# Kernel tuning notes

Hardware: AMD Instinct MI355X
Metric: run time of the kernel (lower is better)

## Reference

```python
import jax, jax.numpy as jnp
import numpy as np
from jax import lax

B, T, D = 1, 2048, 2048
H, KVH, HD = 16, 4, 128
BETA = 0.9
ROPE_BASE = 10000.0


def _causal_prefix_ema(x, beta):
    # x: (B, T, D); m_t = beta * m_{t-1} + (1 - beta) * x_t, m_{-1} = 0
    def step(m, xt):
        m = beta * m + (1.0 - beta) * xt
        return m, m
    _, ys = lax.scan(step, jnp.zeros_like(x[:, 0]), jnp.swapaxes(x, 0, 1))
    return jnp.swapaxes(ys, 0, 1)


def _rotate_half(x):
    x1, x2 = jnp.split(x, 2, axis=-1)
    return jnp.concatenate([-x2, x1], axis=-1)


def _rope_cos_sin(t, hd, dtype):
    inv_freq = 1.0 / (ROPE_BASE ** (jnp.arange(0, hd, 2, dtype=jnp.float32) / hd))
    freqs = jnp.arange(t, dtype=jnp.float32)[:, None] * inv_freq[None, :]  # (T, HD/2)
    emb = jnp.concatenate([freqs, freqs], axis=-1)  # (T, HD)
    return jnp.cos(emb).astype(dtype)[None, None], jnp.sin(emb).astype(dtype)[None, None]


def setup_inputs() -> dict:
    key = jax.random.key(0)
    ks = jax.random.split(key, 8)
    std = 0.02
    return {
        "hidden_states": jax.random.normal(ks[0], (B, T, D), jnp.float32),
        "Wq": jax.random.normal(ks[1], (D, H * HD), jnp.float32) * std,
        "Wk": jax.random.normal(ks[2], (D, KVH * HD), jnp.float32) * std,
        "Wv": jax.random.normal(ks[3], (D, KVH * HD), jnp.float32) * std,
        "Wo": jax.random.normal(ks[4], (H * HD, D), jnp.float32) * std,
        "Wr1": jax.random.normal(ks[5], (D, D // 2), jnp.float32) * std,
        "br1": jnp.zeros((D // 2,), jnp.float32),
        "Wr2": jax.random.normal(ks[6], (D // 2, 2), jnp.float32) * std,
        "br2": jnp.zeros((2,), jnp.float32),
    }


def reference(hidden_states, Wq, Wk, Wv, Wo, Wr1, br1, Wr2, br2):
    b, t, d = hidden_states.shape
    q = hidden_states @ Wq  # (B, T, H*HD)

    # multi-level memories: l1 = raw, l2 = causal prefix EMA
    l2 = _causal_prefix_ema(hidden_states, BETA)

    # router MLP on q + softmax over levels
    h = jax.nn.silu(q @ Wr1 + br1)
    lam = jax.nn.softmax(h @ Wr2 + br2, axis=-1)  # (B, T, 2)
    fused = lam[..., 0:1] * hidden_states + lam[..., 1:2] * l2

    # shape to heads
    q_s = q.reshape(b, t, H, HD).transpose(0, 2, 1, 3)                 # (B, H, T, HD)
    k_s = (fused @ Wk).reshape(b, t, KVH, HD).transpose(0, 2, 1, 3)    # (B, KVH, T, HD)
    v_s = (fused @ Wv).reshape(b, t, KVH, HD).transpose(0, 2, 1, 3)

    # RoPE
    cos, sin = _rope_cos_sin(t, HD, q_s.dtype)
    q_s = q_s * cos + _rotate_half(q_s) * sin
    k_s = k_s * cos + _rotate_half(k_s) * sin

    # repeat kv for GQA
    n_rep = H // KVH
    k_s = jnp.repeat(k_s, n_rep, axis=1)
    v_s = jnp.repeat(v_s, n_rep, axis=1)

    # causal SDPA
    scale = 1.0 / jnp.sqrt(jnp.asarray(HD, q_s.dtype))
    scores = jnp.einsum("bhqd,bhkd->bhqk", q_s, k_s) * scale
    causal = jnp.tril(jnp.ones((t, t), dtype=bool))
    scores = jnp.where(causal[None, None], scores, jnp.finfo(scores.dtype).min)
    attn = jax.nn.softmax(scores, axis=-1)
    out = jnp.einsum("bhqk,bhkd->bhqd", attn, v_s)  # (B, H, T, HD)

    out = out.transpose(0, 2, 1, 3).reshape(b, t, H * HD)
    return out @ Wo
```

## Files before the change

### kernel.cpp

```cpp
#include <hip/hip_runtime.h>
#include <hip/hip_bf16.h>

#define T_SEQ 2048
#define D_MODEL 2048
#define NH 16
#define NKVH 4
#define HD 128

typedef __attribute__((ext_vector_type(8))) short bf16x8;
typedef __attribute__((ext_vector_type(4))) float f32x4;

static __device__ __forceinline__ short f32_to_bf16(float f) {
    unsigned u = __float_as_uint(f);
    u += 0x7fffu + ((u >> 16) & 1u);
    return (short)(u >> 16);
}
static __device__ __forceinline__ float bf16_to_f32(short s) {
    return __uint_as_float(((unsigned)(unsigned short)s) << 16);
}
static __device__ __forceinline__ void gl_to_lds16(const void* g, void* l) {
    __builtin_amdgcn_global_load_lds(
        (const __attribute__((address_space(1))) unsigned int*)g,
        (__attribute__((address_space(3))) unsigned int*)l, 16, 0, 0);
}

template<int BN>
__global__ __launch_bounds__(256, 2) void gemm_bt_kernel(
    const short* __restrict__ A, const short* __restrict__ Bt,
    float* __restrict__ Cf, short* __restrict__ Cb,
    int M, int N, int K, const float* __restrict__ bias, int act)
{
    constexpr int NI = BN / 64;
    constexpr int BCH = BN / 32;
    __shared__ short Alds[2][64 * 64];
    __shared__ short Blds[2][BN * 64];

    const int tid = threadIdx.x;
    const int wave = tid >> 6, lane = tid & 63;
    const int l16 = lane & 15, quad = lane >> 4;
    const int wn = wave * (BN / 4);
    const int m0 = blockIdx.y * 64, n0 = blockIdx.x * BN;
    const int niter = K >> 6;

    f32x4 acc[4][NI] = {};

    #pragma unroll
    for (int p = 0; p < 2; ++p) {
        int li = p * 256 + tid;
        int row = li >> 3, sc = li & 7;
        gl_to_lds16(A + (size_t)(m0 + row) * K + ((sc ^ (row & 7)) * 8),
                    &Alds[0][(size_t)(p * 256 + wave * 64) * 8]);
    }
    #pragma unroll
    for (int p = 0; p < BCH; ++p) {
        int li = p * 256 + tid;
        int row = li >> 3, sc = li & 7;
        gl_to_lds16(Bt + (size_t)(n0 + row) * K + ((sc ^ (row & 7)) * 8),
                    &Blds[0][(size_t)(p * 256 + wave * 64) * 8]);
    }

    for (int t = 0; t < niter; ++t) {
        asm volatile("s_waitcnt vmcnt(0)\n\ts_barrier" ::: "memory");

        if (t + 1 < niter) {
            int k1 = (t + 1) << 6;
            int nb = (t + 1) & 1;
            #pragma unroll
            for (int p = 0; p < 2; ++p) {
                int li = p * 256 + tid;
                int row = li >> 3, sc = li & 7;
                gl_to_lds16(A + (size_t)(m0 + row) * K + k1 + ((sc ^ (row & 7)) * 8),
                            &Alds[nb][(size_t)(p * 256 + wave * 64) * 8]);
            }
            #pragma unroll
            for (int p = 0; p < BCH; ++p) {
                int li = p * 256 + tid;
                int row = li >> 3, sc = li & 7;
                gl_to_lds16(Bt + (size_t)(n0 + row) * K + k1 + ((sc ^ (row & 7)) * 8),
                            &Blds[nb][(size_t)(p * 256 + wave * 64) * 8]);
            }
        }

        const short* Ab = Alds[t & 1];
        const short* Bb = Blds[t & 1];
        #pragma unroll
        for (int kk = 0; kk < 2; ++kk) {
            bf16x8 a[4], b[NI];
            #pragma unroll
            for (int i = 0; i < 4; ++i)
                a[i] = *(const bf16x8*)
                    &Ab[(size_t)(i * 16 + l16) * 64 + (((kk * 4 + quad) ^ (l16 & 7)) * 8)];
            #pragma unroll
            for (int i = 0; i < NI; ++i)
                b[i] = *(const bf16x8*)
                    &Bb[(size_t)(wn + i * 16 + l16) * 64 + (((kk * 4 + quad) ^ (l16 & 7)) * 8)];
            #pragma unroll
            for (int mi = 0; mi < 4; ++mi)
                #pragma unroll
                for (int ni = 0; ni < NI; ++ni)
                    acc[mi][ni] = __builtin_amdgcn_mfma_f32_16x16x32_bf16(
                        a[mi], b[ni], acc[mi][ni], 0, 0, 0);
        }
    }

    #pragma unroll
    for (int mi = 0; mi < 4; ++mi) {
        #pragma unroll
        for (int ni = 0; ni < NI; ++ni) {
            int col = n0 + wn + ni * 16 + l16;
            float bv = bias ? bias[col] : 0.0f;
            #pragma unroll
            for (int r = 0; r < 4; ++r) {
                int row = m0 + mi * 16 + quad * 4 + r;
                float x = acc[mi][ni][r] + bv;
                if (act) x = x / (1.0f + __expf(-x));
                size_t o = (size_t)row * N + col;
                if (Cf) Cf[o] = x;
                if (Cb) Cb[o] = f32_to_bf16(x);
            }
        }
    }
}

__global__ __launch_bounds__(256) void transpose_all_kernel(
    const float* __restrict__ Wq, const float* __restrict__ Wk,
    const float* __restrict__ Wv, const float* __restrict__ Wr1,
    const float* __restrict__ Wo, short* __restrict__ Wq_t,
    short* __restrict__ Wkv_t, short* __restrict__ Wr1_t,
    short* __restrict__ Wo_t)
{
    __shared__ float tile[32][33];
    int bx = blockIdx.x;
    const float* src; short* dst; int ld, cb;
    if (bx < 64)       { src = Wq;  dst = Wq_t;  ld = 2048; cb = bx; }
    else if (bx < 80)  { src = Wk;  dst = Wkv_t; ld = 512;  cb = bx - 64; }
    else if (bx < 96)  { src = Wv;  dst = Wkv_t + (size_t)512 * 2048; ld = 512; cb = bx - 80; }
    else if (bx < 128) { src = Wr1; dst = Wr1_t; ld = 1024; cb = bx - 96; }
    else               { src = Wo;  dst = Wo_t;  ld = 2048; cb = bx - 128; }
    int c0 = cb * 32, r0 = blockIdx.y * 32;
    int t = threadIdx.x;
    int r = t >> 3, c4 = (t & 7) * 4;
    float4 v = *(const float4*)&src[(size_t)(r0 + r) * ld + c0 + c4];
    tile[r][c4 + 0] = v.x; tile[r][c4 + 1] = v.y;
    tile[r][c4 + 2] = v.z; tile[r][c4 + 3] = v.w;
    __syncthreads();
    short o[4];
    #pragma unroll
    for (int j = 0; j < 4; ++j) o[j] = f32_to_bf16(tile[c4 + j][r]);
    *(uint2*)&dst[(size_t)(c0 + r) * 2048 + r0 + c4] = *(const uint2*)o;
}

__global__ __launch_bounds__(256) void transpose_bf_kernel(
    const short* __restrict__ src, int ld, short* __restrict__ dst, int ldd)
{
    __shared__ float tile[32][33];
    int r0 = blockIdx.y * 32, c0 = blockIdx.x * 32;
    int x = threadIdx.x & 31, y = threadIdx.x >> 5;
    #pragma unroll
    for (int i = 0; i < 4; ++i)
        tile[y + i * 8][x] = bf16_to_f32(src[(size_t)(r0 + y + i * 8) * ld + c0 + x]);
    __syncthreads();
    #pragma unroll
    for (int i = 0; i < 4; ++i)
        dst[(size_t)(c0 + y + i * 8) * ldd + r0 + x] = f32_to_bf16(tile[x][y + i * 8]);
}

__global__ __launch_bounds__(256) void ema_kernel(const float* __restrict__ hs,
                                                  float* __restrict__ l2,
                                                  short* __restrict__ hs_b)
{
    int d = blockIdx.y * 256 + threadIdx.x;
    int t0 = blockIdx.x * 128;
    int ts = t0 - 192; if (ts < 0) ts = 0;
    float m = 0.0f;
    for (int tb = ts; tb < t0; tb += 16) {
        float buf[16];
        #pragma unroll
        for (int j = 0; j < 16; ++j) buf[j] = hs[(size_t)(tb + j) * D_MODEL + d];
        #pragma unroll
        for (int j = 0; j < 16; ++j) m = 0.9f * m + 0.1f * buf[j];
    }
    for (int tb = t0; tb < t0 + 128; tb += 16) {
        float buf[16];
        #pragma unroll
        for (int j = 0; j < 16; ++j) buf[j] = hs[(size_t)(tb + j) * D_MODEL + d];
        #pragma unroll
        for (int j = 0; j < 16; ++j) hs_b[(size_t)(tb + j) * D_MODEL + d] = f32_to_bf16(buf[j]);
        #pragma unroll
        for (int j = 0; j < 16; ++j) { m = 0.9f * m + 0.1f * buf[j]; buf[j] = m; }
        #pragma unroll
        for (int j = 0; j < 16; ++j) l2[(size_t)(tb + j) * D_MODEL + d] = buf[j];
    }
}

__global__ __launch_bounds__(64) void lam_kernel(
    const short* __restrict__ h, const float* __restrict__ Wr2,
    const float* __restrict__ br2, float* __restrict__ lam)
{
    int t = blockIdx.x;
    int lane = threadIdx.x;
    float z0 = 0.0f, z1 = 0.0f;
    for (int i = lane; i < 1024; i += 64) {
        float hv = bf16_to_f32(h[(size_t)t * 1024 + i]);
        z0 += hv * Wr2[i * 2 + 0];
        z1 += hv * Wr2[i * 2 + 1];
    }
    #pragma unroll
    for (int off = 1; off < 64; off <<= 1) {
        z0 += __shfl_xor(z0, off);
        z1 += __shfl_xor(z1, off);
    }
    if (lane == 0) {
        z0 += br2[0]; z1 += br2[1];
        float mx = fmaxf(z0, z1);
        float e0 = expf(z0 - mx), e1 = expf(z1 - mx);
        float inv = 1.0f / (e0 + e1);
        lam[t * 2 + 0] = e0 * inv;
        lam[t * 2 + 1] = e1 * inv;
    }
}

__global__ void fuse_kernel(const float* __restrict__ hs, const float* __restrict__ l2,
                            const float* __restrict__ lam, short* __restrict__ fused)
{
    int idx = blockIdx.x * blockDim.x + threadIdx.x;
    int t = idx >> 9;
    float a0 = lam[t * 2 + 0], a1 = lam[t * 2 + 1];
    float4 a = ((const float4*)hs)[idx];
    float4 b = ((const float4*)l2)[idx];
    short o[4] = {f32_to_bf16(a0 * a.x + a1 * b.x), f32_to_bf16(a0 * a.y + a1 * b.y),
                  f32_to_bf16(a0 * a.z + a1 * b.z), f32_to_bf16(a0 * a.w + a1 * b.w)};
    *(uint2*)(fused + (size_t)idx * 4) = *(const uint2*)o;
}

__global__ void rope_q_kernel(const short* __restrict__ q, short* __restrict__ qr)
{
    int idx = blockIdx.x * blockDim.x + threadIdx.x;
    int d = idx & 63;
    int h = (idx >> 6) & 15;
    int t = idx >> 10;
    float fr = (float)t * __expf(-(float)d * 0.14391156831212787f);
    float s, c;
    sincosf(fr, &s, &c);
    const float sc = 0.08838834764831845f;
    const short* src = q + (size_t)t * D_MODEL + h * HD;
    float x1 = bf16_to_f32(src[d]) * sc, x2 = bf16_to_f32(src[d + 64]) * sc;
    short* dst = qr + ((size_t)h * T_SEQ + t) * HD;
    dst[d]      = f32_to_bf16(x1 * c - x2 * s);
    dst[d + 64] = f32_to_bf16(x2 * c + x1 * s);
}

__global__ void rope_k_kernel(const short* __restrict__ kv, short* __restrict__ kr)
{
    int idx = blockIdx.x * blockDim.x + threadIdx.x;
    int d = idx & 63;
    int kh = (idx >> 6) & 3;
    int t = idx >> 8;
    float fr = (float)t * __expf(-(float)d * 0.14391156831212787f);
    float s, c;
    sincosf(fr, &s, &c);
    const short* src = kv + (size_t)t * 1024 + kh * HD;
    float x1 = bf16_to_f32(src[d]), x2 = bf16_to_f32(src[d + 64]);
    short* dst = kr + ((size_t)kh * T_SEQ + t) * HD;
    dst[d]      = f32_to_bf16(x1 * c - x2 * s);
    dst[d + 64] = f32_to_bf16(x2 * c + x1 * s);
}

__global__ __launch_bounds__(512, 2) void attn_kernel(
    const short* __restrict__ Qr, const short* __restrict__ Kr,
    const short* __restrict__ Vt, short* __restrict__ Out)
{
    const int h = blockIdx.x;
    const int qt = blockIdx.y;
    const int kvh = h >> 2;
    const int tid = threadIdx.x;
    const int wave = tid >> 6, lane = tid & 63;
    const int l16 = lane & 15, quad = lane >> 4;
    const int wq = wave & 3;
    const int wk = wave >> 2;

    __shared__ __align__(16) char smem[163840];
    short* Klds = (short*)smem;
    short* Vlds = (short*)(smem + 65536);
    short* Plds = (short*)(smem + 131072);

    const short* kbase = Kr + (size_t)kvh * T_SEQ * HD;
    const short* vbase = Vt + (size_t)kvh * HD * T_SEQ;

    const int qbase = qt * 128 + wq * 32;
    const int ko = wk * 64;
    const int n = qt + 1;

    bf16x8 qf[2][4];
    #pragma unroll
    for (int m = 0; m < 2; ++m) {
        const short* qrow = Qr + ((size_t)h * T_SEQ + qbase + m * 16 + l16) * HD;
        #pragma unroll
        for (int kc = 0; kc < 4; ++kc)
            qf[m][kc] = *(const bf16x8*)&qrow[kc * 32 + quad * 8];
    }
    f32x4 o[2][8] = {};
    float lsum[2][4] = {};

    {
        #pragma unroll
        for (int p = 0; p < 4; ++p) {
            int li = p * 512 + tid;
            int row = li >> 4, gs = (li & 15) ^ (row & 15);
            gl_to_lds16(kbase + (size_t)row * HD + gs * 8,
                        &Klds[(size_t)(p * 512 + wave * 64) * 8]);
        }
        #pragma unroll
        for (int p = 0; p < 4; ++p) {
            int li = p * 512 + tid;
            int row = li >> 4, gs = (li & 15) ^ (row & 15);
            gl_to_lds16(vbase + (size_t)row * T_SEQ + gs * 8,
                        &Vlds[(size_t)(p * 512 + wave * 64) * 8]);
        }
    }

    for (int t = 0; t < n; ++t) {
        asm volatile("s_waitcnt vmcnt(0)\n\ts_barrier" ::: "memory");

        if (t + 1 < n) {
            int kv1 = (t + 1) << 7;
            int nb = (t + 1) & 1;
            const short* ks = kbase + (size_t)kv1 * HD;
            #pragma unroll
            for (int p = 0; p < 4; ++p) {
                int li = p * 512 + tid;
                int row = li >> 4, gs = (li & 15) ^ (row & 15);
                gl_to_lds16(ks + (size_t)row * HD + gs * 8,
                            &Klds[(size_t)(nb * 16384 + (p * 512 + wave * 64) * 8)]);
            }
            #pragma unroll
            for (int p = 0; p < 4; ++p) {
                int li = p * 512 + tid;
                int row = li >> 4, gs = (li & 15) ^ (row & 15);
                gl_to_lds16(vbase + (size_t)row * T_SEQ + kv1 + gs * 8,
                            &Vlds[(size_t)(nb * 16384 + (p * 512 + wave * 64) * 8)]);
            }
        }

        const short* Kb = Klds + (size_t)(t & 1) * 16384;
        const short* Vb = Vlds + (size_t)(t & 1) * 16384;

        f32x4 s[2][4];
        #pragma unroll
        for (int m = 0; m < 2; ++m)
            #pragma unroll
            for (int ni = 0; ni < 4; ++ni) s[m][ni] = (f32x4){0, 0, 0, 0};
        __builtin_amdgcn_s_setprio(1);
        #pragma unroll
        for (int ni = 0; ni < 4; ++ni)
            #pragma unroll
            for (int kc = 0; kc < 4; ++kc) {
                bf16x8 b = *(const bf16x8*)
                    &Kb[(size_t)(ko + ni * 16 + l16) * 128 + (((kc * 4 + quad) ^ l16) * 8)];
                s[0][ni] = __builtin_amdgcn_mfma_f32_16x16x32_bf16(qf[0][kc], b, s[0][ni], 0, 0, 0);
                s[1][ni] = __builtin_amdgcn_mfma_f32_16x16x32_bf16(qf[1][kc], b, s[1][ni], 0, 0, 0);
            }
        __builtin_amdgcn_s_setprio(0);

        if (t == n - 1) {
            int kvg0 = (t << 7) + ko;
            #pragma unroll
            for (int m = 0; m < 2; ++m)
                #pragma unroll
                for (int ni = 0; ni < 4; ++ni) {
                    int kvg = kvg0 + ni * 16 + l16;
                    #pragma unroll
                    for (int r = 0; r < 4; ++r) {
                        int qg = qbase + m * 16 + quad * 4 + r;
                        float p = (kvg <= qg) ? __expf(s[m][ni][r]) : 0.0f;
                        lsum[m][r] += p;
                        int prow = quad * 4 + r, pcol = ni * 16 + l16;
                        Plds[wave * 2048 + (m * 16 + prow) * 64 +
                             (((pcol >> 3) ^ (prow & 7)) * 8) + (pcol & 7)] = f32_to_bf16(p);
                    }
                }
        } else {
            #pragma unroll
            for (int m = 0; m < 2; ++m)
                #pragma unroll
                for (int ni = 0; ni < 4; ++ni)
                    #pragma unroll
                    for (int r = 0; r < 4; ++r) {
                        float p = __expf(s[m][ni][r]);
                        lsum[m][r] += p;
                        int prow = quad * 4 + r, pcol = ni * 16 + l16;
                        Plds[wave * 2048 + (m * 16 + prow) * 64 +
                             (((pcol >> 3) ^ (prow & 7)) * 8) + (pcol & 7)] = f32_to_bf16(p);
                    }
        }
        asm volatile("s_waitcnt lgkmcnt(0)" ::: "memory");

        __builtin_amdgcn_s_setprio(1);
        #pragma unroll
        for (int kc = 0; kc < 2; ++kc) {
            bf16x8 pa0 = *(const bf16x8*)
                &Plds[wave * 2048 + l16 * 64 + (((kc * 4 + quad) ^ (l16 & 7)) * 8)];
            bf16x8 pa1 = *(const bf16x8*)
                &Plds[wave * 2048 + (16 + l16) * 64 + (((kc * 4 + quad) ^ (l16 & 7)) * 8)];
            #pragma unroll
            for (int d8 = 0; d8 < 8; ++d8) {
                bf16x8 b = *(const bf16x8*)
                    &Vb[(size_t)(d8 * 16 + l16) * 128 +
                        (((wk * 8 + kc * 4 + quad) ^ l16) * 8)];
                o[0][d8] = __builtin_amdgcn_mfma_f32_16x16x32_bf16(pa0, b, o[0][d8], 0, 0, 0);
                o[1][d8] = __builtin_amdgcn_mfma_f32_16x16x32_bf16(pa1, b, o[1][d8], 0, 0, 0);
            }
        }
        __builtin_amdgcn_s_setprio(0);
    }

    __syncthreads();
    float* Ox = (float*)smem;
    float* Lx = (float*)(smem + 67584);
    if (wk) {
        #pragma unroll
        for (int m = 0; m < 2; ++m)
            #pragma unroll
            for (int d8 = 0; d8 < 8; ++d8)
                #pragma unroll
                for (int r = 0; r < 4; ++r)
                    Ox[(wq * 32 + m * 16 + quad * 4 + r) * 132 + d8 * 16 + l16] = o[m][d8][r];
        #pragma unroll
        for (int m = 0; m < 2; ++m)
            #pragma unroll
            for (int r = 0; r < 4; ++r)
                Lx[(wq * 32 + m * 16 + quad * 4 + r) * 16 + l16] = lsum[m][r];
    }
    __syncthreads();
    if (!wk) {
        #pragma unroll
        for (int m = 0; m < 2; ++m)
            #pragma unroll
            for (int d8 = 0; d8 < 8; ++d8)
                #pragma unroll
                for (int r = 0; r < 4; ++r)
                    o[m][d8][r] += Ox[(wq * 32 + m * 16 + quad * 4 + r) * 132 + d8 * 16 + l16];
        #pragma unroll
        for (int m = 0; m < 2; ++m)
            #pragma unroll
            for (int r = 0; r < 4; ++r) {
                lsum[m][r] += Lx[(wq * 32 + m * 16 + quad * 4 + r) * 16 + l16];
                #pragma unroll
                for (int off = 1; off < 16; off <<= 1)
                    lsum[m][r] += __shfl_xor(lsum[m][r], off);
                lsum[m][r] = 1.0f / lsum[m][r];
            }
        #pragma unroll
        for (int m = 0; m < 2; ++m)
            #pragma unroll
            for (int d8 = 0; d8 < 8; ++d8)
                #pragma unroll
                for (int r = 0; r < 4; ++r) {
                    int row = qbase + m * 16 + quad * 4 + r;
                    Out[(size_t)row * D_MODEL + h * HD + d8 * 16 + l16] =
                        f32_to_bf16(o[m][d8][r] * lsum[m][r]);
                }
    }
}

extern "C" void kernel_launch(void* const* d_in, const int* in_sizes, int n_in,
                              void* d_out, int out_size, void* d_ws, size_t ws_size,
                              hipStream_t stream)
{
    const float* hs  = (const float*)d_in[0];
    const float* Wq  = (const float*)d_in[1];
    const float* Wk  = (const float*)d_in[2];
    const float* Wv  = (const float*)d_in[3];
    const float* Wo  = (const float*)d_in[4];
    const float* Wr1 = (const float*)d_in[5];
    const float* br1 = (const float*)d_in[6];
    const float* Wr2 = (const float*)d_in[7];
    const float* br2 = (const float*)d_in[8];
    float* out = (float*)d_out;

    char* w = (char*)d_ws;
    const size_t MB = 1u << 20;
    float* l2_f     = (float*)(w + 0 * MB);
    short* hs_bf    = (short*)(w + 16 * MB);
    short* Wq_t     = (short*)(w + 24 * MB);
    short* Wkv_t    = (short*)(w + 32 * MB);
    short* Wr1_t    = (short*)(w + 36 * MB);
    short* Wo_t     = (short*)(w + 40 * MB);
    short* q_bf     = (short*)(w + 48 * MB);
    short* h_bf     = (short*)(w + 56 * MB);
    short* fused_bf = (short*)(w + 60 * MB);
    short* kv_bf    = (short*)(w + 68 * MB);
    short* qr       = (short*)(w + 72 * MB);
    short* kr       = (short*)(w + 80 * MB);
    short* vr       = (short*)(w + 82 * MB);
    float* lam_f    = (float*)(w + 84 * MB);
    short* attn_bf  = hs_bf;

    transpose_all_kernel<<<dim3(192, 64), 256, 0, stream>>>(
        Wq, Wk, Wv, Wr1, Wo, Wq_t, Wkv_t, Wr1_t, Wo_t);

    ema_kernel<<<dim3(T_SEQ / 128, D_MODEL / 256), 256, 0, stream>>>(hs, l2_f, hs_bf);

    gemm_bt_kernel<128><<<dim3(16, 32), 256, 0, stream>>>(
        hs_bf, Wq_t, nullptr, q_bf, 2048, 2048, 2048, nullptr, 0);

    gemm_bt_kernel<64><<<dim3(16, 32), 256, 0, stream>>>(
        q_bf, Wr1_t, nullptr, h_bf, 2048, 1024, 2048, br1, 1);

    lam_kernel<<<T_SEQ, 64, 0, stream>>>(h_bf, Wr2, br2, lam_f);

    fuse_kernel<<<(T_SEQ * D_MODEL / 4) / 256, 256, 0, stream>>>(hs, l2_f, lam_f, fused_bf);

    gemm_bt_kernel<64><<<dim3(16, 32), 256, 0, stream>>>(
        fused_bf, Wkv_t, nullptr, kv_bf, 2048, 1024, 2048, nullptr, 0);

    rope_q_kernel<<<(T_SEQ * NH * 64) / 256, 256, 0, stream>>>(q_bf, qr);
    rope_k_kernel<<<(T_SEQ * NKVH * 64) / 256, 256, 0, stream>>>(kv_bf, kr);
    transpose_bf_kernel<<<dim3(16, 64), 256, 0, stream>>>(kv_bf + 512, 1024, vr, 2048);

    attn_kernel<<<dim3(NH, 16), 512, 0, stream>>>(qr, kr, vr, attn_bf);

    gemm_bt_kernel<128><<<dim3(16, 32), 256, 0, stream>>>(
        attn_bf, Wo_t, out, nullptr, 2048, 2048, 2048, nullptr, 0);
}
```

Before: 321.6 us.

## Balance causal attention by pairing 64-row query tiles per block

The attention kernel now gives each block two 64-row query tiles, y and 31-y, in sequence, so the causal work per block is roughly equal. Previously each block handled a single 128-row tile, so the work per block grew with the tile index. Waves are reorganised as 2 query groups by 4 KV splits. Partial O and row sums from 3 waves are reduced through LDS, and the LDS footprint is reduced. The cost is that even tiles compute half-masked 128-wide KV blocks, and there is extra reduction and a barrier between phases.

```diff
diff --git a/kernel.cpp b/kernel.cpp
--- a/kernel.cpp
+++ b/kernel.cpp
@@ -271,15 +271,15 @@
     const short* __restrict__ Vt, short* __restrict__ Out)
 {
     const int h = blockIdx.x;
-    const int qt = blockIdx.y;
+    const int y = blockIdx.y;
     const int kvh = h >> 2;
     const int tid = threadIdx.x;
     const int wave = tid >> 6, lane = tid & 63;
     const int l16 = lane & 15, quad = lane >> 4;
-    const int wq = wave & 3;
-    const int wk = wave >> 2;
-
-    __shared__ __align__(16) char smem[163840];
+    const int wq = wave & 1;
+    const int wk = wave >> 1;
+
+    __shared__ __align__(16) char smem[147456];
     short* Klds = (short*)smem;
     short* Vlds = (short*)(smem + 65536);
     short* Plds = (short*)(smem + 131072);
@@ -287,179 +287,190 @@
     const short* kbase = Kr + (size_t)kvh * T_SEQ * HD;
     const short* vbase = Vt + (size_t)kvh * HD * T_SEQ;
 
-    const int qbase = qt * 128 + wq * 32;
-    const int ko = wk * 64;
-    const int n = qt + 1;
-
-    bf16x8 qf[2][4];
-    #pragma unroll
-    for (int m = 0; m < 2; ++m) {
-        const short* qrow = Qr + ((size_t)h * T_SEQ + qbase + m * 16 + l16) * HD;
-        #pragma unroll
-        for (int kc = 0; kc < 4; ++kc)
-            qf[m][kc] = *(const bf16x8*)&qrow[kc * 32 + quad * 8];
-    }
-    f32x4 o[2][8] = {};
-    float lsum[2][4] = {};
-
-    {
-        #pragma unroll
-        for (int p = 0; p < 4; ++p) {
-            int li = p * 512 + tid;
-            int row = li >> 4, gs = (li & 15) ^ (row & 15);
-            gl_to_lds16(kbase + (size_t)row * HD + gs * 8,
-                        &Klds[(size_t)(p * 512 + wave * 64) * 8]);
-        }
-        #pragma unroll
-        for (int p = 0; p < 4; ++p) {
-            int li = p * 512 + tid;
-            int row = li >> 4, gs = (li & 15) ^ (row & 15);
-            gl_to_lds16(vbase + (size_t)row * T_SEQ + gs * 8,
-                        &Vlds[(size_t)(p * 512 + wave * 64) * 8]);
-        }
-    }
-
-    for (int t = 0; t < n; ++t) {
-        asm volatile("s_waitcnt vmcnt(0)\n\ts_barrier" ::: "memory");
-
-        if (t + 1 < n) {
-            int kv1 = (t + 1) << 7;
-            int nb = (t + 1) & 1;
-            const short* ks = kbase + (size_t)kv1 * HD;
+    #pragma unroll 1
+    for (int ph = 0; ph < 2; ++ph) {
+        const int qt32 = ph ? (31 - y) : y;
+        const int qbase = qt32 * 64 + wq * 32;
+        const int n = (qt32 >> 1) + 1;
+        const int ko = wk * 32;
+
+        bf16x8 qf[2][4];
+        #pragma unroll
+        for (int m = 0; m < 2; ++m) {
+            const short* qrow = Qr + ((size_t)h * T_SEQ + qbase + m * 16 + l16) * HD;
+            #pragma unroll
+            for (int kc = 0; kc < 4; ++kc)
+                qf[m][kc] = *(const bf16x8*)&qrow[kc * 32 + quad * 8];
+        }
+        f32x4 o[2][8] = {};
+        float lsum[2][4] = {};
+
+        __syncthreads();
+
+        {
             #pragma unroll
             for (int p = 0; p < 4; ++p) {
                 int li = p * 512 + tid;
                 int row = li >> 4, gs = (li & 15) ^ (row & 15);
-                gl_to_lds16(ks + (size_t)row * HD + gs * 8,
-                            &Klds[(size_t)(nb * 16384 + (p * 512 + wave * 64) * 8)]);
+                gl_to_lds16(kbase + (size_t)row * HD + gs * 8,
+                            &Klds[(size_t)(p * 512 + wave * 64) * 8]);
             }
             #pragma unroll
             for (int p = 0; p < 4; ++p) {
                 int li = p * 512 + tid;
                 int row = li >> 4, gs = (li & 15) ^ (row & 15);
-                gl_to_lds16(vbase + (size_t)row * T_SEQ + kv1 + gs * 8,
-                            &Vlds[(size_t)(nb * 16384 + (p * 512 + wave * 64) * 8)]);
-            }
-        }
-
-        const short* Kb = Klds + (size_t)(t & 1) * 16384;
-        const short* Vb = Vlds + (size_t)(t & 1) * 16384;
-
-        f32x4 s[2][4];
-        #pragma unroll
-        for (int m = 0; m < 2; ++m)
-            #pragma unroll
-            for (int ni = 0; ni < 4; ++ni) s[m][ni] = (f32x4){0, 0, 0, 0};
-        __builtin_amdgcn_s_setprio(1);
-        #pragma unroll
-        for (int ni = 0; ni < 4; ++ni)
-            #pragma unroll
-            for (int kc = 0; kc < 4; ++kc) {
-                bf16x8 b = *(const bf16x8*)
-                    &Kb[(size_t)(ko + ni * 16 + l16) * 128 + (((kc * 4 + quad) ^ l16) * 8)];
-                s[0][ni] = __builtin_amdgcn_mfma_f32_16x16x32_bf16(qf[0][kc], b, s[0][ni], 0, 0, 0);
-                s[1][ni] = __builtin_amdgcn_mfma_f32_16x16x32_bf16(qf[1][kc], b, s[1][ni], 0, 0, 0);
-            }
-        __builtin_amdgcn_s_setprio(0);
-
-        if (t == n - 1) {
-            int kvg0 = (t << 7) + ko;
+                gl_to_lds16(vbase + (size_t)row * T_SEQ + gs * 8,
+                            &Vlds[(size_t)(p * 512 + wave * 64) * 8]);
+            }
+        }
+
+        for (int t = 0; t < n; ++t) {
+            asm volatile("s_waitcnt vmcnt(0)\n\ts_barrier" ::: "memory");
+
+            if (t + 1 < n) {
+                int kv1 = (t + 1) << 7;
+                int nb = (t + 1) & 1;
+                const short* ks = kbase + (size_t)kv1 * HD;
+                #pragma unroll
+                for (int p = 0; p < 4; ++p) {
+                    int li = p * 512 + tid;
+                    int row = li >> 4, gs = (li & 15) ^ (row & 15);
+                    gl_to_lds16(ks + (size_t)row * HD + gs * 8,
+                                &Klds[(size_t)(nb * 16384 + (p * 512 + wave * 64) * 8)]);
+                }
+                #pragma unroll
+                for (int p = 0; p < 4; ++p) {
+                    int li = p * 512 + tid;
+                    int row = li >> 4, gs = (li & 15) ^ (row & 15);
+                    gl_to_lds16(vbase + (size_t)row * T_SEQ + kv1 + gs * 8,
+                                &Vlds[(size_t)(nb * 16384 + (p * 512 + wave * 64) * 8)]);
+                }
+            }
+
+            const short* Kb = Klds + (size_t)(t & 1) * 16384;
+            const short* Vb = Vlds + (size_t)(t & 1) * 16384;
+
+            f32x4 s[2][2];
             #pragma unroll
             for (int m = 0; m < 2; ++m)
                 #pragma unroll
-                for (int ni = 0; ni < 4; ++ni) {
-                    int kvg = kvg0 + ni * 16 + l16;
+                for (int ni = 0; ni < 2; ++ni) s[m][ni] = (f32x4){0, 0, 0, 0};
+            __builtin_amdgcn_s_setprio(1);
+            #pragma unroll
+            for (int ni = 0; ni < 2; ++ni)
+                #pragma unroll
+                for (int kc = 0; kc < 4; ++kc) {
+                    bf16x8 b = *(const bf16x8*)
+                        &Kb[(size_t)(ko + ni * 16 + l16) * 128 + (((kc * 4 + quad) ^ l16) * 8)];
+                    s[0][ni] = __builtin_amdgcn_mfma_f32_16x16x32_bf16(qf[0][kc], b, s[0][ni], 0, 0, 0);
+                    s[1][ni] = __builtin_amdgcn_mfma_f32_16x16x32_bf16(qf[1][kc], b, s[1][ni], 0, 0, 0);
+                }
+            __builtin_amdgcn_s_setprio(0);
+
+            if (t == n - 1) {
+                int kvg0 = (t << 7) + ko;
+                #pragma unroll
+                for (int m = 0; m < 2; ++m)
+                    #pragma unroll
+                    for (int ni = 0; ni < 2; ++ni) {
+                        int kvg = kvg0 + ni * 16 + l16;
+                        #pragma unroll
+                        for (int r = 0; r < 4; ++r) {
+                            int qg = qbase + m * 16 + quad * 4 + r;
+                            float p = (kvg <= qg) ? __expf(s[m][ni][r]) : 0.0f;
+                            lsum[m][r] += p;
+                            int prow = quad * 4 + r, pcol = ni * 16 + l16;
+                            Plds[wave * 1024 + (m * 16 + prow) * 32 +
+                                 (((pcol >> 3) ^ (prow & 3)) * 8) + (pcol & 7)] = f32_to_bf16(p);
+                        }
+                    }
+            } else {
+                #pragma unroll
+                for (int m = 0; m < 2; ++m)
+                    #pragma unroll
+                    for (int ni = 0; ni < 2; ++ni)
+                        #pragma unroll
+                        for (int r = 0; r < 4; ++r) {
+                            float p = __expf(s[m][ni][r]);
+                            lsum[m][r] += p;
+                            int prow = quad * 4 + r, pcol = ni * 16 + l16;
+                            Plds[wave * 1024 + (m * 16 + prow) * 32 +
+                                 (((pcol >> 3) ^ (prow & 3)) * 8) + (pcol & 7)] = f32_to_bf16(p);
+                        }
+            }
+            asm volatile("s_waitcnt lgkmcnt(0)" ::: "memory");
+
+            __builtin_amdgcn_s_setprio(1);
+            {
+                bf16x8 pa0 = *(const bf16x8*)
+                    &Plds[wave * 1024 + l16 * 32 + ((quad ^ (l16 & 3)) * 8)];
+                bf16x8 pa1 = *(const bf16x8*)
+                    &Plds[wave * 1024 + (16 + l16) * 32 + ((quad ^ (l16 & 3)) * 8)];
+                #pragma unroll
+                for (int d8 = 0; d8 < 8; ++d8) {
+                    bf16x8 b = *(const bf16x8*)
+                        &Vb[(size_t)(d8 * 16 + l16) * 128 +
+                            (((wk * 4 + quad) ^ l16) * 8)];
+                    o[0][d8] = __builtin_amdgcn_mfma_f32_16x16x32_bf16(pa0, b, o[0][d8], 0, 0, 0);
+                    o[1][d8] = __builtin_amdgcn_mfma_f32_16x16x32_bf16(pa1, b, o[1][d8], 0, 0, 0);
+                }
+            }
+            __builtin_amdgcn_s_setprio(0);
+        }
+
+        __syncthreads();
+        float* Ox = (float*)smem;
+        float* Lx = (float*)(smem + 101376);
+        if (wk) {
+            int base = (wq * 3 + wk - 1) * 32;
+            #pragma unroll
+            for (int m = 0; m < 2; ++m)
+                #pragma unroll
+                for (int d8 = 0; d8 < 8; ++d8)
+                    #pragma unroll
+                    for (int r = 0; r < 4; ++r)
+                        Ox[(base + m * 16 + quad * 4 + r) * 132 + d8 * 16 + l16] = o[m][d8][r];
+            #pragma unroll
+            for (int m = 0; m < 2; ++m)
+                #pragma unroll
+                for (int r = 0; r < 4; ++r)
+                    Lx[(base + m * 16 + quad * 4 + r) * 16 + l16] = lsum[m][r];
+        }
+        __syncthreads();
+        if (wk == 0) {
+            #pragma unroll
+            for (int j = 0; j < 3; ++j)
+                #pragma unroll
+                for (int m = 0; m < 2; ++m)
+                    #pragma unroll
+                    for (int d8 = 0; d8 < 8; ++d8)
+                        #pragma unroll
+                        for (int r = 0; r < 4; ++r)
+                            o[m][d8][r] += Ox[((wq * 3 + j) * 32 + m * 16 + quad * 4 + r) * 132
+                                              + d8 * 16 + l16];
+            #pragma unroll
+            for (int m = 0; m < 2; ++m)
+                #pragma unroll
+                for (int r = 0; r < 4; ++r) {
+                    #pragma unroll
+                    for (int j = 0; j < 3; ++j)
+                        lsum[m][r] += Lx[((wq * 3 + j) * 32 + m * 16 + quad * 4 + r) * 16 + l16];
+                    #pragma unroll
+                    for (int off = 1; off < 16; off <<= 1)
+                        lsum[m][r] += __shfl_xor(lsum[m][r], off);
+                    lsum[m][r] = 1.0f / lsum[m][r];
+                }
+            #pragma unroll
+            for (int m = 0; m < 2; ++m)
+                #pragma unroll
+                for (int d8 = 0; d8 < 8; ++d8)
                     #pragma unroll
                     for (int r = 0; r < 4; ++r) {
-                        int qg = qbase + m * 16 + quad * 4 + r;
-                        float p = (kvg <= qg) ? __expf(s[m][ni][r]) : 0.0f;
-                        lsum[m][r] += p;
-                        int prow = quad * 4 + r, pcol = ni * 16 + l16;
-                        Plds[wave * 2048 + (m * 16 + prow) * 64 +
-                             (((pcol >> 3) ^ (prow & 7)) * 8) + (pcol & 7)] = f32_to_bf16(p);
+                        int row = qbase + m * 16 + quad * 4 + r;
+                        Out[(size_t)row * D_MODEL + h * HD + d8 * 16 + l16] =
+                            f32_to_bf16(o[m][d8][r] * lsum[m][r]);
                     }
-                }
-        } else {
-            #pragma unroll
-            for (int m = 0; m < 2; ++m)
-                #pragma unroll
-                for (int ni = 0; ni < 4; ++ni)
-                    #pragma unroll
-                    for (int r = 0; r < 4; ++r) {
-                        float p = __expf(s[m][ni][r]);
-                        lsum[m][r] += p;
-                        int prow = quad * 4 + r, pcol = ni * 16 + l16;
-                        Plds[wave * 2048 + (m * 16 + prow) * 64 +
-                             (((pcol >> 3) ^ (prow & 7)) * 8) + (pcol & 7)] = f32_to_bf16(p);
-                    }
-        }
-        asm volatile("s_waitcnt lgkmcnt(0)" ::: "memory");
-
-        __builtin_amdgcn_s_setprio(1);
-        #pragma unroll
-        for (int kc = 0; kc < 2; ++kc) {
-            bf16x8 pa0 = *(const bf16x8*)
-                &Plds[wave * 2048 + l16 * 64 + (((kc * 4 + quad) ^ (l16 & 7)) * 8)];
-            bf16x8 pa1 = *(const bf16x8*)
-                &Plds[wave * 2048 + (16 + l16) * 64 + (((kc * 4 + quad) ^ (l16 & 7)) * 8)];
-            #pragma unroll
-            for (int d8 = 0; d8 < 8; ++d8) {
-                bf16x8 b = *(const bf16x8*)
-                    &Vb[(size_t)(d8 * 16 + l16) * 128 +
-                        (((wk * 8 + kc * 4 + quad) ^ l16) * 8)];
-                o[0][d8] = __builtin_amdgcn_mfma_f32_16x16x32_bf16(pa0, b, o[0][d8], 0, 0, 0);
-                o[1][d8] = __builtin_amdgcn_mfma_f32_16x16x32_bf16(pa1, b, o[1][d8], 0, 0, 0);
-            }
-        }
-        __builtin_amdgcn_s_setprio(0);
-    }
-
-    __syncthreads();
-    float* Ox = (float*)smem;
-    float* Lx = (float*)(smem + 67584);
-    if (wk) {
-        #pragma unroll
-        for (int m = 0; m < 2; ++m)
-            #pragma unroll
-            for (int d8 = 0; d8 < 8; ++d8)
-                #pragma unroll
-                for (int r = 0; r < 4; ++r)
-                    Ox[(wq * 32 + m * 16 + quad * 4 + r) * 132 + d8 * 16 + l16] = o[m][d8][r];
-        #pragma unroll
-        for (int m = 0; m < 2; ++m)
-            #pragma unroll
-            for (int r = 0; r < 4; ++r)
-                Lx[(wq * 32 + m * 16 + quad * 4 + r) * 16 + l16] = lsum[m][r];
-    }
-    __syncthreads();
-    if (!wk) {
-        #pragma unroll
-        for (int m = 0; m < 2; ++m)
-            #pragma unroll
-            for (int d8 = 0; d8 < 8; ++d8)
-                #pragma unroll
-                for (int r = 0; r < 4; ++r)
-                    o[m][d8][r] += Ox[(wq * 32 + m * 16 + quad * 4 + r) * 132 + d8 * 16 + l16];
-        #pragma unroll
-        for (int m = 0; m < 2; ++m)
-            #pragma unroll
-            for (int r = 0; r < 4; ++r) {
-                lsum[m][r] += Lx[(wq * 32 + m * 16 + quad * 4 + r) * 16 + l16];
-                #pragma unroll
-                for (int off = 1; off < 16; off <<= 1)
-                    lsum[m][r] += __shfl_xor(lsum[m][r], off);
-                lsum[m][r] = 1.0f / lsum[m][r];
-            }
-        #pragma unroll
-        for (int m = 0; m < 2; ++m)
-            #pragma unroll
-            for (int d8 = 0; d8 < 8; ++d8)
-                #pragma unroll
-                for (int r = 0; r < 4; ++r) {
-                    int row = qbase + m * 16 + quad * 4 + r;
-                    Out[(size_t)row * D_MODEL + h * HD + d8 * 16 + l16] =
-                        f32_to_bf16(o[m][d8][r] * lsum[m][r]);
-                }
+        }
     }
 }
 
```

Result: faster. 314.7 us (-2.2%).
